# Performance work log

Hardware: AMD Instinct MI355X
Metric: run time of the kernel (lower is better)

Reference implementation:

```python
import jax, jax.numpy as jnp
import numpy as np

DIM = 1024
HEADS = 8
DIM_HEAD = 64
DIM_INNER = HEADS * DIM_HEAD  # 512


def setup_inputs() -> dict:
    key = jax.random.key(0)
    k1, k2, k3, k4 = jax.random.split(key, 4)
    x = jax.random.normal(k1, (1, 4096, DIM), dtype=jnp.float32)
    gamma = jnp.ones((DIM,), dtype=jnp.float32)
    w_qkv = jax.random.normal(k2, (DIM, 3 * DIM_INNER), dtype=jnp.float32) * (DIM ** -0.5)
    w_out = jax.random.normal(k3, (DIM_INNER, DIM), dtype=jnp.float32) * (DIM_INNER ** -0.5)
    return {"x": x, "gamma": gamma, "w_qkv": w_qkv, "w_out": w_out}


def _rmsnorm(x, gamma):
    # F.normalize(x, dim=-1) * sqrt(dim) * gamma
    norm = jnp.sqrt(jnp.sum(x * x, axis=-1, keepdims=True))
    x = x / jnp.maximum(norm, 1e-12)
    return x * (DIM ** 0.5) * gamma


def reference(x, gamma, w_qkv, w_out):
    b, n, _ = x.shape
    h, d = HEADS, DIM_HEAD
    normed = _rmsnorm(x, gamma)
    qkv = normed @ w_qkv  # [b, n, 3*h*d]
    qkv = qkv.reshape(b, n, 3, h, d)
    q = jnp.transpose(qkv[:, :, 0], (0, 2, 1, 3))  # b h n d
    k = jnp.transpose(qkv[:, :, 1], (0, 2, 1, 3))
    v = jnp.transpose(qkv[:, :, 2], (0, 2, 1, 3))
    # default_attention (faithful: scales q by d**0.5 as in source)
    q = q * (d ** 0.5)
    sim = jnp.einsum('bhid,bhjd->bhij', q, k)
    mask_value = -jnp.finfo(sim.dtype).max
    causal_mask = jnp.triu(jnp.ones((n, n), dtype=bool), 1)
    sim = jnp.where(causal_mask, mask_value, sim)
    attn = jax.nn.softmax(sim, axis=-1)
    out = jnp.einsum('bhij,bhjd->bhid', attn, v)  # b h n d
    out = jnp.transpose(out, (0, 2, 1, 3)).reshape(b, n, h * d)
    return out @ w_out  # [b, n, dim]
```

## Files before the change

### kernel.cpp

```cpp
#include <hip/hip_runtime.h>
#include <math.h>

#define SEQ 4096
#define DIM 1024
#define HEADS 8
#define DINNER 512
#define QKVW 1536
#define PAD 80
#define CHUNK 16

typedef unsigned short u16;
typedef __attribute__((ext_vector_type(8))) short s8v;
typedef __attribute__((ext_vector_type(4))) float f4v;
#define MFMA(a, b, c) __builtin_amdgcn_mfma_f32_16x16x32_bf16(a, b, c, 0, 0, 0)

__device__ __forceinline__ u16 f2bf(float f) {
    unsigned u = __float_as_uint(f);
    u += 0x7fff + ((u >> 16) & 1);
    return (u16)(u >> 16);
}
__device__ __forceinline__ float bf2f(u16 b) { return __uint_as_float(((unsigned)b) << 16); }

__device__ __forceinline__ void gload16(const u16* g, u16* l) {
    __builtin_amdgcn_global_load_lds(
        (const __attribute__((address_space(1))) unsigned int*)g,
        (__attribute__((address_space(3))) unsigned int*)l, 16, 0, 0);
}

__device__ __forceinline__ int base16(int qt) {
    int a = qt >> 4, b = qt & 15;
    return 8 * a * (a + 1) + b * (a + 1);
}
__device__ __forceinline__ float* po_sel(int T, float* pd, float* pw) {
    return (T < 1024) ? pd + (size_t)T * 4096 : pw + (size_t)(T - 1024) * 4096;
}

__global__ __launch_bounds__(256) void rmsnorm_split(const float* __restrict__ x,
                                                     const float* __restrict__ gamma,
                                                     u16* __restrict__ hi,
                                                     u16* __restrict__ lo) {
    __shared__ float red[4];
    const int row = blockIdx.x, t = threadIdx.x;
    const float* xr = x + (size_t)row * DIM;
    float v[4];
    float ss = 0.f;
#pragma unroll
    for (int i = 0; i < 4; ++i) { v[i] = xr[t + i * 256]; ss += v[i] * v[i]; }
#pragma unroll
    for (int off = 32; off >= 1; off >>= 1) ss += __shfl_xor(ss, off, 64);
    if ((t & 63) == 0) red[t >> 6] = ss;
    __syncthreads();
    float scale = 32.0f / fmaxf(sqrtf(red[0] + red[1] + red[2] + red[3]), 1e-12f);
#pragma unroll
    for (int i = 0; i < 4; ++i) {
        int c = t + i * 256;
        float y = v[i] * scale * gamma[c];
        u16 h = f2bf(y);
        hi[(size_t)row * DIM + c] = h;
        lo[(size_t)row * DIM + c] = f2bf(y - bf2f(h));
    }
}

__global__ __launch_bounds__(256) void transpose_split(const float* __restrict__ in,
                                                       u16* __restrict__ hi,
                                                       u16* __restrict__ lo,
                                                       int R, int C, int want_lo) {
    __shared__ float tile[64][65];
    const int c0 = blockIdx.x * 64, r0 = blockIdx.y * 64;
    const int t = threadIdx.x, col = t & 63, rb = t >> 6;
#pragma unroll
    for (int j = 0; j < 16; ++j)
        tile[rb + j * 4][col] = in[(size_t)(r0 + rb + j * 4) * C + c0 + col];
    __syncthreads();
#pragma unroll
    for (int j = 0; j < 16; ++j) {
        int cc = rb + j * 4;
        float v = tile[col][cc];
        size_t oi = (size_t)(c0 + cc) * R + r0 + col;
        u16 h = f2bf(v);
        hi[oi] = h;
        if (want_lo) lo[oi] = f2bf(v - bf2f(h));
    }
}

__global__ __launch_bounds__(256) void gemm_qkv_128(
    const u16* __restrict__ Ah, const u16* __restrict__ Al,
    const u16* __restrict__ Bh, const u16* __restrict__ Bl,
    u16* __restrict__ qh, u16* __restrict__ ql,
    u16* __restrict__ kh, u16* __restrict__ kl, u16* __restrict__ vtp) {
    __shared__ __align__(16) u16 AsH[128 * 64], AsL[128 * 64];
    __shared__ __align__(16) u16 BsH[64 * 64], BsL[64 * 64];
    const int t = threadIdx.x;
    const int bn = blockIdx.x * 64, bm = blockIdx.y * 128;
    const int w = t >> 6, lane = t & 63, m = lane & 15, q = lane >> 4;
    const int wr = w >> 1, wc = w & 1;
    f4v acc[4][2];
#pragma unroll
    for (int i = 0; i < 4; ++i)
#pragma unroll
        for (int j = 0; j < 2; ++j) acc[i][j] = (f4v){0.f, 0.f, 0.f, 0.f};

    for (int k0 = 0; k0 < DIM; k0 += 64) {
        __syncthreads();
#pragma unroll
        for (int i = 0; i < 4; ++i) {
            int idx0 = i * 256 + w * 64;
            int row = (idx0 + lane) >> 3;
            int col = ((lane & 7) * 8) ^ ((row & 7) * 8);
            gload16(&Ah[(size_t)(bm + row) * DIM + k0 + col], &AsH[idx0 * 8]);
            gload16(&Al[(size_t)(bm + row) * DIM + k0 + col], &AsL[idx0 * 8]);
            if (i < 2) {
                gload16(&Bh[(size_t)(bn + row) * DIM + k0 + col], &BsH[idx0 * 8]);
                gload16(&Bl[(size_t)(bn + row) * DIM + k0 + col], &BsL[idx0 * 8]);
            }
        }
        __syncthreads();
#pragma unroll
        for (int kk = 0; kk < 64; kk += 32) {
            s8v a_h[4], a_l[4], b_h[2], b_l[2];
#pragma unroll
            for (int f = 0; f < 4; ++f) {
                int ar = wr * 64 + f * 16 + m;
                int ab = ar * 128 + (((kk + q * 8) * 2) ^ ((ar & 7) << 4));
                a_h[f] = *(const s8v*)((const char*)AsH + ab);
                a_l[f] = *(const s8v*)((const char*)AsL + ab);
            }
#pragma unroll
            for (int f = 0; f < 2; ++f) {
                int br = wc * 32 + f * 16 + m;
                int bb = br * 128 + (((kk + q * 8) * 2) ^ ((br & 7) << 4));
                b_h[f] = *(const s8v*)((const char*)BsH + bb);
                b_l[f] = *(const s8v*)((const char*)BsL + bb);
            }
#pragma unroll
            for (int fm = 0; fm < 4; ++fm)
#pragma unroll
                for (int fn = 0; fn < 2; ++fn) {
                    acc[fm][fn] = MFMA(a_h[fm], b_h[fn], acc[fm][fn]);
                    acc[fm][fn] = MFMA(a_l[fm], b_h[fn], acc[fm][fn]);
                    acc[fm][fn] = MFMA(a_h[fm], b_l[fn], acc[fm][fn]);
                }
        }
    }
    const int region = bn >> 9;
#pragma unroll
    for (int fm = 0; fm < 4; ++fm)
#pragma unroll
        for (int fn = 0; fn < 2; ++fn)
#pragma unroll
            for (int r = 0; r < 4; ++r) {
                int gr = bm + wr * 64 + fm * 16 + q * 4 + r;
                int gc = bn + wc * 32 + fn * 16 + m;
                float v = acc[fm][fn][r];
                if (region == 0) {
                    v *= 8.0f;
                    u16 h = f2bf(v);
                    qh[(size_t)gr * DINNER + gc] = h;
                    ql[(size_t)gr * DINNER + gc] = f2bf(v - bf2f(h));
                } else if (region == 1) {
                    u16 h = f2bf(v);
                    kh[(size_t)gr * DINNER + (gc - 512)] = h;
                    kl[(size_t)gr * DINNER + (gc - 512)] = f2bf(v - bf2f(h));
                } else {
                    vtp[(size_t)(gc - 1024) * SEQ + gr] = f2bf(v);
                }
            }
}

__global__ __launch_bounds__(256) void attn_chunk(
    const u16* __restrict__ qhp, const u16* __restrict__ qlp,
    const u16* __restrict__ kh, const u16* __restrict__ kl,
    const u16* __restrict__ vt,
    float* __restrict__ po_dout, float* __restrict__ po_wqt,
    float* __restrict__ ml) {
    __shared__ u16 KP[64 * PAD], Kl[64 * PAD], Vt[64 * PAD];
    const int t = threadIdx.x;
    const int bx = blockIdx.x;
    const int qt = 63 - (bx >> 2), c = bx & 3, h = blockIdx.y;
    if (c * CHUNK > qt) return;
    const int kt0 = c * CHUNK;
    const int kt1 = (qt < kt0 + CHUNK - 1) ? qt : (kt0 + CHUNK - 1);
    const int w = t >> 6, lane = t & 63, m = lane & 15, g = lane >> 4;

    const size_t qrow = (size_t)(qt * 64 + w * 16 + m) * DINNER + h * 64;
    const s8v qf_h0 = *(const s8v*)&qhp[qrow + g * 8];
    const s8v qf_h1 = *(const s8v*)&qhp[qrow + 32 + g * 8];
    const s8v qf_l0 = *(const s8v*)&qlp[qrow + g * 8];
    const s8v qf_l1 = *(const s8v*)&qlp[qrow + 32 + g * 8];

    f4v o[4] = {{0.f, 0.f, 0.f, 0.f}, {0.f, 0.f, 0.f, 0.f},
                {0.f, 0.f, 0.f, 0.f}, {0.f, 0.f, 0.f, 0.f}};
    float mi_s = -1e30f, li_s = 0.f;

    for (int kt = kt0; kt <= kt1; ++kt) {
        __syncthreads();
#pragma unroll
        for (int i = 0; i < 2; ++i) {
            int c2 = t + i * 256, row = c2 >> 3, ch = (c2 & 7) * 8;
            *(uint4*)&KP[row * PAD + ch] =
                *(const uint4*)&kh[(size_t)(kt * 64 + row) * DINNER + h * 64 + ch];
            *(uint4*)&Kl[row * PAD + ch] =
                *(const uint4*)&kl[(size_t)(kt * 64 + row) * DINNER + h * 64 + ch];
            *(uint4*)&Vt[row * PAD + ch] =
                *(const uint4*)&vt[(size_t)(h * 64 + row) * SEQ + kt * 64 + ch];
        }
        __syncthreads();

        f4v s[4] = {{0.f, 0.f, 0.f, 0.f}, {0.f, 0.f, 0.f, 0.f},
                    {0.f, 0.f, 0.f, 0.f}, {0.f, 0.f, 0.f, 0.f}};
#pragma unroll
        for (int ct = 0; ct < 4; ++ct) {
            s8v bh0 = *(const s8v*)&KP[(ct * 16 + m) * PAD + g * 8];
            s8v bl0 = *(const s8v*)&Kl[(ct * 16 + m) * PAD + g * 8];
            s[ct] = MFMA(bh0, qf_h0, s[ct]);
            s[ct] = MFMA(bh0, qf_l0, s[ct]);
            s[ct] = MFMA(bl0, qf_h0, s[ct]);
            s8v bh1 = *(const s8v*)&KP[(ct * 16 + m) * PAD + 32 + g * 8];
            s8v bl1 = *(const s8v*)&Kl[(ct * 16 + m) * PAD + 32 + g * 8];
            s[ct] = MFMA(bh1, qf_h1, s[ct]);
            s[ct] = MFMA(bh1, qf_l1, s[ct]);
            s[ct] = MFMA(bl1, qf_h1, s[ct]);
        }
        if (kt == qt) {
#pragma unroll
            for (int ct = 0; ct < 4; ++ct)
#pragma unroll
                for (int r = 0; r < 4; ++r)
                    if (ct * 16 + g * 4 + r > w * 16 + m) s[ct][r] = -1e30f;
        }

        float rm = -1e30f;
#pragma unroll
        for (int ct = 0; ct < 4; ++ct)
#pragma unroll
            for (int r = 0; r < 4; ++r) rm = fmaxf(rm, s[ct][r]);
        rm = fmaxf(rm, __shfl_xor(rm, 16, 64));
        rm = fmaxf(rm, __shfl_xor(rm, 32, 64));
        float mn = fmaxf(mi_s, rm);
        float al = __expf(mi_s - mn);
        mi_s = mn;
        float rs = 0.f;
#pragma unroll
        for (int ct = 0; ct < 4; ++ct)
#pragma unroll
            for (int r = 0; r < 4; ++r) {
                s[ct][r] = __expf(s[ct][r] - mn);
                rs += s[ct][r];
            }
        rs += __shfl_xor(rs, 16, 64);
        rs += __shfl_xor(rs, 32, 64);
        li_s = li_s * al + rs;
        float alo[4];
#pragma unroll
        for (int r = 0; r < 4; ++r) alo[r] = __shfl(al, g * 4 + r, 64);

        __syncthreads();
#pragma unroll
        for (int ct = 0; ct < 4; ++ct) {
            unsigned w0 = (unsigned)f2bf(s[ct][0]) | ((unsigned)f2bf(s[ct][1]) << 16);
            unsigned w1 = (unsigned)f2bf(s[ct][2]) | ((unsigned)f2bf(s[ct][3]) << 16);
            *(uint2*)&KP[(w * 16 + m) * PAD + ct * 16 + g * 4] = make_uint2(w0, w1);
        }
#pragma unroll
        for (int ct = 0; ct < 4; ++ct)
#pragma unroll
            for (int r = 0; r < 4; ++r) o[ct][r] *= alo[r];
#pragma unroll
        for (int kk = 0; kk < 64; kk += 32) {
            s8v ap = *(const s8v*)&KP[(w * 16 + m) * PAD + kk + g * 8];
#pragma unroll
            for (int ct = 0; ct < 4; ++ct) {
                s8v bv = *(const s8v*)&Vt[(ct * 16 + m) * PAD + kk + g * 8];
                o[ct] = MFMA(ap, bv, o[ct]);
            }
        }
    }

    const int T = h * 160 + base16(qt) + c;
    float* po = po_sel(T, po_dout, po_wqt);
#pragma unroll
    for (int ct = 0; ct < 4; ++ct)
#pragma unroll
        for (int r = 0; r < 4; ++r)
            po[(size_t)(w * 16 + g * 4 + r) * 64 + ct * 16 + m] = o[ct][r];
    if (g == 0) {
        ml[(size_t)T * 128 + w * 16 + m] = mi_s;
        ml[(size_t)T * 128 + 64 + w * 16 + m] = li_s;
    }
}

__global__ __launch_bounds__(256) void attn_merge(
    float* __restrict__ po_dout, float* __restrict__ po_wqt,
    const float* __restrict__ ml, u16* __restrict__ atto) {
    const int qt = blockIdx.x, h = blockIdx.y;
    const int nc = (qt >> 4) + 1;
    const int t = threadIdx.x, col = t & 63, rg = t >> 6;
    const int T0 = h * 160 + base16(qt);
    for (int j = 0; j < 16; ++j) {
        int row = rg * 16 + j;
        float mv[4], lv[4], M = -1e30f;
#pragma unroll 4
        for (int cc = 0; cc < 4; ++cc)
            if (cc < nc) {
                mv[cc] = ml[(size_t)(T0 + cc) * 128 + row];
                lv[cc] = ml[(size_t)(T0 + cc) * 128 + 64 + row];
                M = fmaxf(M, mv[cc]);
            }
        float acc = 0.f, den = 0.f;
#pragma unroll 4
        for (int cc = 0; cc < 4; ++cc)
            if (cc < nc) {
                const float* po = po_sel(T0 + cc, po_dout, po_wqt);
                float wg = __expf(mv[cc] - M);
                den += lv[cc] * wg;
                acc += wg * po[(size_t)row * 64 + col];
            }
        atto[(size_t)(qt * 64 + row) * DINNER + h * 64 + col] = f2bf(acc / den);
    }
}

__global__ __launch_bounds__(256) void attn_mfma(
    const u16* __restrict__ qh, const u16* __restrict__ ql,
    const u16* __restrict__ kh, const u16* __restrict__ kl,
    const u16* __restrict__ vt, u16* __restrict__ atto) {
    __shared__ u16 Qh[64 * PAD], Ql[64 * PAD], KP[64 * PAD], Kl[64 * PAD], Vt[64 * PAD];
    const int t = threadIdx.x;
    const int qt = blockIdx.x, h = blockIdx.y;
    const int w = t >> 6, lane = t & 63, m = lane & 15, q = lane >> 4;

#pragma unroll
    for (int i = 0; i < 2; ++i) {
        int c = t + i * 256, row = c >> 3, ch = (c & 7) * 8;
        *(uint4*)&Qh[row * PAD + ch] =
            *(const uint4*)&qh[(size_t)(qt * 64 + row) * DINNER + h * 64 + ch];
        *(uint4*)&Ql[row * PAD + ch] =
            *(const uint4*)&ql[(size_t)(qt * 64 + row) * DINNER + h * 64 + ch];
    }

    f4v o[4] = {{0.f, 0.f, 0.f, 0.f}, {0.f, 0.f, 0.f, 0.f},
                {0.f, 0.f, 0.f, 0.f}, {0.f, 0.f, 0.f, 0.f}};
    float mi[4] = {-1e30f, -1e30f, -1e30f, -1e30f};
    float li[4] = {0.f, 0.f, 0.f, 0.f};

    for (int kt = 0; kt <= qt; ++kt) {
        __syncthreads();
#pragma unroll
        for (int i = 0; i < 2; ++i) {
            int c = t + i * 256, row = c >> 3, ch = (c & 7) * 8;
            *(uint4*)&KP[row * PAD + ch] =
                *(const uint4*)&kh[(size_t)(kt * 64 + row) * DINNER + h * 64 + ch];
            *(uint4*)&Kl[row * PAD + ch] =
                *(const uint4*)&kl[(size_t)(kt * 64 + row) * DINNER + h * 64 + ch];
            *(uint4*)&Vt[row * PAD + ch] =
                *(const uint4*)&vt[(size_t)(h * 64 + row) * SEQ + kt * 64 + ch];
        }
        __syncthreads();

        f4v s[4] = {{0.f, 0.f, 0.f, 0.f}, {0.f, 0.f, 0.f, 0.f},
                    {0.f, 0.f, 0.f, 0.f}, {0.f, 0.f, 0.f, 0.f}};
#pragma unroll
        for (int kk = 0; kk < 64; kk += 32) {
            s8v ah = *(const s8v*)&Qh[(w * 16 + m) * PAD + kk + q * 8];
            s8v al = *(const s8v*)&Ql[(w * 16 + m) * PAD + kk + q * 8];
#pragma unroll
            for (int ct = 0; ct < 4; ++ct) {
                s8v bh = *(const s8v*)&KP[(ct * 16 + m) * PAD + kk + q * 8];
                s8v bl = *(const s8v*)&Kl[(ct * 16 + m) * PAD + kk + q * 8];
                s[ct] = MFMA(ah, bh, s[ct]);
                s[ct] = MFMA(al, bh, s[ct]);
                s[ct] = MFMA(ah, bl, s[ct]);
            }
        }
        if (kt == qt) {
#pragma unroll
            for (int ct = 0; ct < 4; ++ct)
#pragma unroll
                for (int r = 0; r < 4; ++r)
                    if (ct * 16 + m > w * 16 + q * 4 + r) s[ct][r] = -1e30f;
        }

        float alpha[4];
#pragma unroll
        for (int r = 0; r < 4; ++r) {
            float rm = fmaxf(fmaxf(s[0][r], s[1][r]), fmaxf(s[2][r], s[3][r]));
#pragma unroll
            for (int off = 8; off >= 1; off >>= 1) rm = fmaxf(rm, __shfl_xor(rm, off, 64));
            float mn = fmaxf(mi[r], rm);
            alpha[r] = __expf(mi[r] - mn);
            mi[r] = mn;
            float rs = 0.f;
#pragma unroll
            for (int ct = 0; ct < 4; ++ct) {
                s[ct][r] = __expf(s[ct][r] - mn);
                rs += s[ct][r];
            }
#pragma unroll
            for (int off = 8; off >= 1; off >>= 1) rs += __shfl_xor(rs, off, 64);
            li[r] = li[r] * alpha[r] + rs;
        }

        __syncthreads();
#pragma unroll
        for (int ct = 0; ct < 4; ++ct)
#pragma unroll
            for (int r = 0; r < 4; ++r) {
                KP[(w * 16 + q * 4 + r) * PAD + ct * 16 + m] = f2bf(s[ct][r]);
                o[ct][r] *= alpha[r];
            }
#pragma unroll
        for (int kk = 0; kk < 64; kk += 32) {
            s8v ap = *(const s8v*)&KP[(w * 16 + m) * PAD + kk + q * 8];
#pragma unroll
            for (int ct = 0; ct < 4; ++ct) {
                s8v bv = *(const s8v*)&Vt[(ct * 16 + m) * PAD + kk + q * 8];
                o[ct] = MFMA(ap, bv, o[ct]);
            }
        }
    }

#pragma unroll
    for (int r = 0; r < 4; ++r) {
        float inv = 1.0f / li[r];
#pragma unroll
        for (int ct = 0; ct < 4; ++ct)
            atto[(size_t)(qt * 64 + w * 16 + q * 4 + r) * DINNER + h * 64 + ct * 16 + m] =
                f2bf(o[ct][r] * inv);
    }
}

__global__ __launch_bounds__(256) void gemm_out_bf16(const u16* __restrict__ A,
                                                     const u16* __restrict__ Bt,
                                                     float* __restrict__ C) {
    __shared__ u16 As[64 * PAD], Bs[64 * PAD];
    const int t = threadIdx.x;
    const int bn = blockIdx.x * 64, bm = blockIdx.y * 64;
    const int w = t >> 6, lane = t & 63, m = lane & 15, q = lane >> 4;
    f4v acc[4] = {{0.f, 0.f, 0.f, 0.f}, {0.f, 0.f, 0.f, 0.f},
                  {0.f, 0.f, 0.f, 0.f}, {0.f, 0.f, 0.f, 0.f}};
    for (int k0 = 0; k0 < DINNER; k0 += 64) {
        __syncthreads();
#pragma unroll
        for (int i = 0; i < 2; ++i) {
            int c = t + i * 256, row = c >> 3, ch = (c & 7) * 8;
            *(uint4*)&As[row * PAD + ch] = *(const uint4*)&A[(size_t)(bm + row) * DINNER + k0 + ch];
            *(uint4*)&Bs[row * PAD + ch] = *(const uint4*)&Bt[(size_t)(bn + row) * DINNER + k0 + ch];
        }
        __syncthreads();
#pragma unroll
        for (int kk = 0; kk < 64; kk += 32) {
            s8v a = *(const s8v*)&As[(w * 16 + m) * PAD + kk + q * 8];
#pragma unroll
            for (int ct = 0; ct < 4; ++ct) {
                s8v b = *(const s8v*)&Bs[(ct * 16 + m) * PAD + kk + q * 8];
                acc[ct] = MFMA(a, b, acc[ct]);
            }
        }
    }
#pragma unroll
    for (int ct = 0; ct < 4; ++ct)
#pragma unroll
        for (int r = 0; r < 4; ++r)
            C[(size_t)(bm + w * 16 + q * 4 + r) * DIM + bn + ct * 16 + m] = acc[ct][r];
}

extern "C" void kernel_launch(void* const* d_in, const int* in_sizes, int n_in,
                              void* d_out, int out_size, void* d_ws, size_t ws_size,
                              hipStream_t stream) {
    const float* x     = (const float*)d_in[0];
    const float* gamma = (const float*)d_in[1];
    const float* w_qkv = (const float*)d_in[2];
    const float* w_out = (const float*)d_in[3];
    float* out = (float*)d_out;

    u16* nh = (u16*)d_out;
    u16* nl = nh + (size_t)SEQ * DIM;

    u16* p = (u16*)d_ws;
    u16* wqt_h = p; p += (size_t)QKVW * DIM;
    u16* wqt_l = p; p += (size_t)QKVW * DIM;
    u16* wot   = p; p += (size_t)DIM * DINNER;
    u16* qh = p; p += (size_t)SEQ * DINNER;
    u16* ql = p; p += (size_t)SEQ * DINNER;
    u16* kh = p; p += (size_t)SEQ * DINNER;
    u16* kl = p; p += (size_t)SEQ * DINNER;
    u16* vt = p; p += (size_t)DINNER * SEQ;
    u16* atto = p; p += (size_t)SEQ * DINNER;

    float* po_dout = (float*)d_out;
    float* po_wqt  = (float*)wqt_h;
    float* ml      = (float*)p;
    const size_t need = (size_t)((char*)(ml + (size_t)1280 * 128) - (char*)d_ws);
    const bool split = ws_size >= need;

    transpose_split<<<dim3(QKVW / 64, DIM / 64), 256, 0, stream>>>(w_qkv, wqt_h, wqt_l,
                                                                   DIM, QKVW, 1);
    transpose_split<<<dim3(DIM / 64, DINNER / 64), 256, 0, stream>>>(w_out, wot, nullptr,
                                                                     DINNER, DIM, 0);
    rmsnorm_split<<<SEQ, 256, 0, stream>>>(x, gamma, nh, nl);
    gemm_qkv_128<<<dim3(QKVW / 64, SEQ / 128), 256, 0, stream>>>(nh, nl, wqt_h, wqt_l,
                                                                 qh, ql, kh, kl, vt);
    if (split) {
        attn_chunk<<<dim3(256, HEADS), 256, 0, stream>>>(qh, ql, kh, kl, vt,
                                                         po_dout, po_wqt, ml);
        attn_merge<<<dim3(SEQ / 64, HEADS), 256, 0, stream>>>(po_dout, po_wqt, ml, atto);
    } else {
        attn_mfma<<<dim3(SEQ / 64, HEADS), 256, 0, stream>>>(qh, ql, kh, kl, vt, atto);
    }
    gemm_out_bf16<<<dim3(DIM / 64, SEQ / 64), 256, 0, stream>>>(atto, wot, out);
}
```

Before: 296.3 us.

## Double-buffer K/V tiles with async global-to-LDS loads and XOR swizzle

Replaces the synchronous register-staged load of each K-high, K-low and V^T tile with global_load_lds direct copies into a double-buffered shared-memory ring. The next tile is prefetched while the current one is computed. The padded LDS layout becomes an unpadded 64x64 layout with an XOR swizzle on 16-byte chunks to avoid bank conflicts, and the P matrix is written into the current K-high buffer. The aim is to hide global load latency behind MFMA work, at the cost of double the LDS footprint and reliance on correct wait ordering for the async LDS loads.

Result: no change. 293.9 us (-0.8%).

```diff
diff --git a/kernel.cpp b/kernel.cpp
--- a/kernel.cpp
+++ b/kernel.cpp
@@ -173,7 +173,7 @@
     const u16* __restrict__ vt,
     float* __restrict__ po_dout, float* __restrict__ po_wqt,
     float* __restrict__ ml) {
-    __shared__ u16 KP[64 * PAD], Kl[64 * PAD], Vt[64 * PAD];
+    __shared__ __align__(16) u16 KH[2][64 * 64], KL[2][64 * 64], VT[2][64 * 64];
     const int t = threadIdx.x;
     const int bx = blockIdx.x;
     const int qt = 63 - (bx >> 2), c = bx & 3, h = blockIdx.y;
@@ -188,35 +188,57 @@
     const s8v qf_l0 = *(const s8v*)&qlp[qrow + g * 8];
     const s8v qf_l1 = *(const s8v*)&qlp[qrow + 32 + g * 8];
 
+    const int sg0a = w * 64, sg0b = 256 + w * 64;
+    const int srowa = (sg0a + lane) >> 3, srowb = (sg0b + lane) >> 3;
+    const int sca = ((lane & 7) ^ (srowa & 7)) * 8;
+    const int scb = ((lane & 7) ^ (srowb & 7)) * 8;
+
     f4v o[4] = {{0.f, 0.f, 0.f, 0.f}, {0.f, 0.f, 0.f, 0.f},
                 {0.f, 0.f, 0.f, 0.f}, {0.f, 0.f, 0.f, 0.f}};
     float mi_s = -1e30f, li_s = 0.f;
 
+    {
+        const u16* kr = &kh[(size_t)(kt0 * 64) * DINNER + h * 64];
+        const u16* lr = &kl[(size_t)(kt0 * 64) * DINNER + h * 64];
+        const u16* vr = &vt[(size_t)(h * 64) * SEQ + kt0 * 64];
+        gload16(kr + (size_t)srowa * DINNER + sca, &KH[0][sg0a * 8]);
+        gload16(kr + (size_t)srowb * DINNER + scb, &KH[0][sg0b * 8]);
+        gload16(lr + (size_t)srowa * DINNER + sca, &KL[0][sg0a * 8]);
+        gload16(lr + (size_t)srowb * DINNER + scb, &KL[0][sg0b * 8]);
+        gload16(vr + (size_t)srowa * SEQ + sca, &VT[0][sg0a * 8]);
+        gload16(vr + (size_t)srowb * SEQ + scb, &VT[0][sg0b * 8]);
+    }
+    __syncthreads();
+
+    int cur = 0;
     for (int kt = kt0; kt <= kt1; ++kt) {
-        __syncthreads();
-#pragma unroll
-        for (int i = 0; i < 2; ++i) {
-            int c2 = t + i * 256, row = c2 >> 3, ch = (c2 & 7) * 8;
-            *(uint4*)&KP[row * PAD + ch] =
-                *(const uint4*)&kh[(size_t)(kt * 64 + row) * DINNER + h * 64 + ch];
-            *(uint4*)&Kl[row * PAD + ch] =
-                *(const uint4*)&kl[(size_t)(kt * 64 + row) * DINNER + h * 64 + ch];
-            *(uint4*)&Vt[row * PAD + ch] =
-                *(const uint4*)&vt[(size_t)(h * 64 + row) * SEQ + kt * 64 + ch];
-        }
-        __syncthreads();
-
+        if (kt < kt1) {
+            int nb = cur ^ 1;
+            const u16* kr = &kh[(size_t)((kt + 1) * 64) * DINNER + h * 64];
+            const u16* lr = &kl[(size_t)((kt + 1) * 64) * DINNER + h * 64];
+            const u16* vr = &vt[(size_t)(h * 64) * SEQ + (kt + 1) * 64];
+            gload16(kr + (size_t)srowa * DINNER + sca, &KH[nb][sg0a * 8]);
+            gload16(kr + (size_t)srowb * DINNER + scb, &KH[nb][sg0b * 8]);
+            gload16(lr + (size_t)srowa * DINNER + sca, &KL[nb][sg0a * 8]);
+            gload16(lr + (size_t)srowb * DINNER + scb, &KL[nb][sg0b * 8]);
+            gload16(vr + (size_t)srowa * SEQ + sca, &VT[nb][sg0a * 8]);
+            gload16(vr + (size_t)srowb * SEQ + scb, &VT[nb][sg0b * 8]);
+        }
+
+        const char* KHc = (const char*)KH[cur];
+        const char* KLc = (const char*)KL[cur];
         f4v s[4] = {{0.f, 0.f, 0.f, 0.f}, {0.f, 0.f, 0.f, 0.f},
                     {0.f, 0.f, 0.f, 0.f}, {0.f, 0.f, 0.f, 0.f}};
 #pragma unroll
         for (int ct = 0; ct < 4; ++ct) {
-            s8v bh0 = *(const s8v*)&KP[(ct * 16 + m) * PAD + g * 8];
-            s8v bl0 = *(const s8v*)&Kl[(ct * 16 + m) * PAD + g * 8];
+            int rr = ct * 16 + m, rb = rr * 128, sw = (rr & 7) << 4;
+            s8v bh0 = *(const s8v*)(KHc + rb + ((g * 16) ^ sw));
+            s8v bl0 = *(const s8v*)(KLc + rb + ((g * 16) ^ sw));
             s[ct] = MFMA(bh0, qf_h0, s[ct]);
             s[ct] = MFMA(bh0, qf_l0, s[ct]);
             s[ct] = MFMA(bl0, qf_h0, s[ct]);
-            s8v bh1 = *(const s8v*)&KP[(ct * 16 + m) * PAD + 32 + g * 8];
-            s8v bl1 = *(const s8v*)&Kl[(ct * 16 + m) * PAD + 32 + g * 8];
+            s8v bh1 = *(const s8v*)(KHc + rb + ((64 + g * 16) ^ sw));
+            s8v bl1 = *(const s8v*)(KLc + rb + ((64 + g * 16) ^ sw));
             s[ct] = MFMA(bh1, qf_h1, s[ct]);
             s[ct] = MFMA(bh1, qf_l1, s[ct]);
             s[ct] = MFMA(bl1, qf_h1, s[ct]);
@@ -255,25 +277,31 @@
         for (int r = 0; r < 4; ++r) alo[r] = __shfl(al, g * 4 + r, 64);
 
         __syncthreads();
+
+        const int pr = w * 16 + m, pb = pr * 128, psw = (pr & 7) << 4;
 #pragma unroll
         for (int ct = 0; ct < 4; ++ct) {
             unsigned w0 = (unsigned)f2bf(s[ct][0]) | ((unsigned)f2bf(s[ct][1]) << 16);
             unsigned w1 = (unsigned)f2bf(s[ct][2]) | ((unsigned)f2bf(s[ct][3]) << 16);
-            *(uint2*)&KP[(w * 16 + m) * PAD + ct * 16 + g * 4] = make_uint2(w0, w1);
+            *(uint2*)((char*)KH[cur] + pb + ((ct * 32 + g * 8) ^ psw)) = make_uint2(w0, w1);
         }
 #pragma unroll
         for (int ct = 0; ct < 4; ++ct)
 #pragma unroll
             for (int r = 0; r < 4; ++r) o[ct][r] *= alo[r];
 #pragma unroll
-        for (int kk = 0; kk < 64; kk += 32) {
-            s8v ap = *(const s8v*)&KP[(w * 16 + m) * PAD + kk + g * 8];
+        for (int kk = 0; kk < 2; ++kk) {
+            s8v ap = *(const s8v*)((const char*)KH[cur] + pb + ((kk * 64 + g * 16) ^ psw));
 #pragma unroll
             for (int ct = 0; ct < 4; ++ct) {
-                s8v bv = *(const s8v*)&Vt[(ct * 16 + m) * PAD + kk + g * 8];
+                int vr2 = ct * 16 + m;
+                s8v bv = *(const s8v*)((const char*)VT[cur] + vr2 * 128 +
+                                       ((kk * 64 + g * 16) ^ ((vr2 & 7) << 4)));
                 o[ct] = MFMA(ap, bv, o[ct]);
             }
         }
+        __syncthreads();
+        cur ^= 1;
     }
 
     const int T = h * 160 + base16(qt) + c;
```
